# Optimization experiments

Measured on AMD Instinct MI355X. Metric: run time of the kernel, lower is better.

The kernel has to match this reference:

```python
import jax, jax.numpy as jnp
import numpy as np

N, E, B = 10000, 20000, 500
H, NODE_D, EDGE_D, L = 64, 11, 5, 3
BN_EPS = 1e-5
STEPS = 3  # Set2Set processing steps


def setup_inputs() -> dict:
    key = jax.random.key(0)
    ks = jax.random.split(key, 16)
    s = lambda k, shape, fan: (jax.random.normal(k, shape, jnp.float32) / np.sqrt(fan)).astype(jnp.float32)
    p = {}
    p["x"] = jax.random.normal(ks[0], (N, NODE_D), jnp.float32)
    p["edge_index"] = jax.random.randint(ks[1], (2, E), 0, N)
    p["edge_attr"] = jax.random.uniform(ks[2], (E, EDGE_D), dtype=jnp.float32)
    p["batch"] = jnp.sort(jax.random.randint(ks[3], (N,), 0, B))
    # node encoder
    p["W_enc"] = s(ks[4], (NODE_D, H), NODE_D); p["b_enc"] = jnp.zeros((H,), jnp.float32)
    # per-layer NNConv block params (stacked over L layers)
    p["eW1"] = s(ks[5], (L, EDGE_D, H), EDGE_D); p["eb1"] = jnp.zeros((L, H), jnp.float32)
    p["eW2"] = s(ks[6], (L, H, H * H), H);       p["eb2"] = jnp.zeros((L, H * H), jnp.float32)
    p["root"] = s(ks[7], (L, H, H), H);          p["cbias"] = jnp.zeros((L, H), jnp.float32)
    p["gamma"] = jnp.ones((L, H), jnp.float32);  p["beta"] = jnp.zeros((L, H), jnp.float32)
    # Set2Set LSTM (input 2H, hidden H)
    p["Wih"] = s(ks[8], (4 * H, 2 * H), 2 * H); p["Whh"] = s(ks[9], (4 * H, H), H)
    p["bih"] = jnp.zeros((4 * H,), jnp.float32); p["bhh"] = jnp.zeros((4 * H,), jnp.float32)
    p["hW1"] = s(ks[10], (2 * H, H), 2 * H);   p["hb1"] = jnp.zeros((H,), jnp.float32)
    p["hW2"] = s(ks[11], (H, H // 2), H);      p["hb2"] = jnp.zeros((H // 2,), jnp.float32)
    p["hW3"] = s(ks[12], (H // 2, 1), H // 2); p["hb3"] = jnp.zeros((1,), jnp.float32)
    return p


def _forward(x, edge_attr, W_enc, b_enc, eW1, eb1, eW2, eb2, root, cbias, gamma, beta,
             Wih, Whh, bih, bhh, hW1, hb1, hW2, hb2, hW3, hb3, edge_index, batch):
    src, dst = edge_index[0], edge_index[1]
    # in-degree for mean aggregation (0-degree nodes -> 0 output, clamp avoids /0)
    deg = jax.ops.segment_sum(jnp.ones((E,), jnp.float32), dst, num_segments=N)
    deg = jnp.maximum(deg, 1.0)[:, None]

    h = jax.nn.relu(x @ W_enc + b_enc)  # [N, H]

    for l in range(L):
        residual = h
        # edge MLP -> per-edge [H, H] weight matrix
        e1 = jax.nn.relu(edge_attr @ eW1[l] + eb1[l])          # [E, H]
        W = (e1 @ eW2[l] + eb2[l]).reshape(E, H, H)            # [E, H, H]
        msg = jnp.einsum('eh,eho->eo', h[src], W)              # per-edge matvec
        agg = jax.ops.segment_sum(msg, dst, num_segments=N) / deg
        h = agg + h @ root[l] + cbias[l]                       # NNConv (root + bias)
        # BatchNorm1d (training-mode batch stats, biased var), eval-mode dropout (no-op)
        mu = jnp.mean(h, axis=0)
        var = jnp.mean((h - mu) ** 2, axis=0)
        h = (h - mu) * jax.lax.rsqrt(var + BN_EPS) * gamma[l] + beta[l]
        h = jax.nn.relu(h) + residual

    # Set2Set readout
    q_star = jnp.zeros((B, 2 * H), jnp.float32)
    hl = jnp.zeros((B, H), jnp.float32)
    cl = jnp.zeros((B, H), jnp.float32)
    for _ in range(STEPS):
        gates = q_star @ Wih.T + bih + hl @ Whh.T + bhh
        i, f, g, o = jnp.split(gates, 4, axis=1)
        cl = jax.nn.sigmoid(f) * cl + jax.nn.sigmoid(i) * jnp.tanh(g)
        hl = jax.nn.sigmoid(o) * jnp.tanh(cl)
        q = hl                                                  # [B, H]
        e = jnp.sum(h * q[batch], axis=-1)                      # [N]
        m = jax.ops.segment_max(e, batch, num_segments=B)
        ex = jnp.exp(e - m[batch])
        sden = jax.ops.segment_sum(ex, batch, num_segments=B)
        a = ex / sden[batch]                                    # per-graph softmax
        r = jax.ops.segment_sum(a[:, None] * h, batch, num_segments=B)
        q_star = jnp.concatenate([q, r], axis=1)

    # head
    z = jax.nn.relu(q_star @ hW1 + hb1)
    z = jax.nn.relu(z @ hW2 + hb2)
    out = z @ hW3 + hb3
    return out.reshape(-1)  # [B]


def reference(x, edge_index, edge_attr, batch, W_enc, b_enc, eW1, eb1, eW2, eb2, root,
              cbias, gamma, beta, Wih, Whh, bih, bhh, hW1, hb1, hW2, hb2, hW3, hb3):
    return _forward(x, edge_attr, W_enc, b_enc, eW1, eb1, eW2, eb2, root, cbias, gamma,
                    beta, Wih, Whh, bih, bhh, hW1, hb1, hW2, hb2, hW3, hb3,
                    edge_index, batch)
```

## Files before the change

### kernel.cpp

```cpp
#include <hip/hip_runtime.h>
#include <math.h>

#define ND 11
#define ED 5
#define NL 3
#define NSTEPS 3
#define BN_EPS 1e-5f
#define NSLAB 32
#define CAP 256

typedef _Float16 half8 __attribute__((ext_vector_type(8)));
typedef float f32x4 __attribute__((ext_vector_type(4)));

__device__ __forceinline__ float sigm(float x) { return 1.0f / (1.0f + expf(-x)); }

__global__ __launch_bounds__(256) void k_setup(
    const float* __restrict__ x, const float* __restrict__ Wenc,
    const float* __restrict__ benc, float* __restrict__ h0,
    _Float16* __restrict__ hh, int N,
    const int* __restrict__ dst, float* __restrict__ deg, int E,
    const int* __restrict__ batch, int* __restrict__ ptr, int B,
    const float* __restrict__ Wih, const float* __restrict__ Whh,
    const float* __restrict__ bih, const float* __restrict__ bhh,
    float* __restrict__ WihT, float* __restrict__ WhhT, float* __restrict__ gbias,
    const float* __restrict__ w2, const float* __restrict__ b2,
    _Float16* __restrict__ w2P, float* __restrict__ zp, long NZ,
    int nbEnc, int nbDeg, int nbPtr, int nbPackW, int nbPack3) {
  int bid = blockIdx.x;
  const int tid = threadIdx.x;
  if (bid < nbEnc) {
    int idx = bid * 256 + tid;
    if (idx < N * 64) {
      int n = idx >> 6, j = idx & 63;
      float acc = benc[j];
#pragma unroll
      for (int i = 0; i < ND; ++i) acc = fmaf(x[n * ND + i], Wenc[i * 64 + j], acc);
      float v = fmaxf(acc, 0.0f);
      h0[idx] = v;
      hh[idx] = (_Float16)v;
    }
    return;
  }
  bid -= nbEnc;
  if (bid < nbDeg) {
    int e = bid * 256 + tid;
    if (e < E) atomicAdd(&deg[dst[e]], 1.0f);
    return;
  }
  bid -= nbDeg;
  if (bid < nbPtr) {
    int n = bid * 256 + tid;
    if (n < N) {
      int b = batch[n];
      int pb = (n == 0) ? -1 : batch[n - 1];
      for (int g = pb + 1; g <= b; ++g) ptr[g] = n;
      if (n == N - 1)
        for (int g = b + 1; g <= B; ++g) ptr[g] = N;
    }
    return;
  }
  bid -= nbPtr;
  if (bid < nbPackW) {
    int idx = bid * 256 + tid;
    if (idx < 128 * 256) {
      int i = idx >> 8, g = idx & 255;
      WihT[i * 256 + g] = Wih[g * 128 + i];
    } else if (idx < 192 * 256) {
      int j = idx - 128 * 256;
      int i = j >> 8, g = j & 255;
      WhhT[i * 256 + g] = Whh[g * 64 + i];
    } else if (idx < 192 * 256 + 256) {
      int g = idx - 192 * 256;
      gbias[g] = bih[g] + bhh[g];
    }
    return;
  }
  bid -= nbPackW;
  if (bid < nbPack3) {
    int lay = bid / 130;
    int idx = (bid % 130) * 256 + tid;
    int l = idx & 63;
    int f = (idx >> 6) & 7;
    int s = idx >> 9;
    int nf = f >> 1, kf = f & 1;
    const float* srow = (s < 64) ? (w2 + (size_t)lay * 64 * 4096 + (size_t)s * 4096)
                                 : (b2 + (size_t)lay * 4096);
    int o = nf * 16 + (l & 15);
    int hb = kf * 32 + (l >> 4) * 8;
    half8 v;
#pragma unroll
    for (int j = 0; j < 8; ++j) v[j] = (_Float16)srow[(hb + j) * 64 + o];
    *(half8*)(w2P + ((size_t)lay * 65 * 8 * 64 + idx) * 8) = v;
    return;
  }
  bid -= nbPack3;
  {
    long i4 = ((long)bid * 256 + tid) * 4;
    if (i4 + 3 < NZ) *(float4*)(zp + i4) = make_float4(0.f, 0.f, 0.f, 0.f);
    else for (; i4 < NZ; ++i4) zp[i4] = 0.f;
  }
}

__global__ void k_zdeg(float* __restrict__ deg, int N) {
  int i = blockIdx.x * blockDim.x + threadIdx.x;
  if (i < N) deg[i] = 0.f;
}

__global__ __launch_bounds__(256) void k_scan(const float* __restrict__ deg,
                                              int* __restrict__ dptr,
                                              int* __restrict__ cursor, int N) {
  __shared__ int wsum[4];
  __shared__ int s_carry;
  const int tid = threadIdx.x, lane = tid & 63, w = tid >> 6;
  if (tid == 0) s_carry = 0;
  __syncthreads();
  for (int base = 0; base < N; base += 1024) {
    int n0 = base + tid * 4;
    int v[4];
    int s = 0;
#pragma unroll
    for (int i = 0; i < 4; ++i) { v[i] = (n0 + i < N) ? (int)deg[n0 + i] : 0; s += v[i]; }
    int sc = s;
#pragma unroll
    for (int off = 1; off < 64; off <<= 1) {
      int t = __shfl_up(sc, off);
      if (lane >= off) sc += t;
    }
    if (lane == 63) wsum[w] = sc;
    __syncthreads();
    int wpre = 0;
    for (int ww = 0; ww < w; ++ww) wpre += wsum[ww];
    int excl = s_carry + wpre + sc - s;
#pragma unroll
    for (int i = 0; i < 4; ++i) {
      if (n0 + i < N) { dptr[n0 + i] = excl; cursor[n0 + i] = excl; }
      excl += v[i];
    }
    __syncthreads();
    if (tid == 255) s_carry += wsum[0] + wsum[1] + wsum[2] + wsum[3];
    __syncthreads();
  }
  if (threadIdx.x == 0) dptr[N] = s_carry;
}

__global__ void k_fill(const int* __restrict__ dst, const int* __restrict__ src,
                       int* __restrict__ cursor, int* __restrict__ perm,
                       int* __restrict__ srcP, int* __restrict__ dstP, int E) {
  int e = blockIdx.x * blockDim.x + threadIdx.x;
  if (e < E) {
    int d = dst[e];
    int slot = atomicAdd(&cursor[d], 1);
    perm[slot] = e;
    srcP[slot] = src[e];
    dstP[slot] = d;
  }
}

__global__ __launch_bounds__(256) void k_hmat(
    const float* __restrict__ hn, const float* __restrict__ hp,
    const float* __restrict__ slab, const float* __restrict__ gm,
    const float* __restrict__ bt, float* __restrict__ hout,
    _Float16* __restrict__ hh, int N) {
  __shared__ float stats[128];
  const int tid = threadIdx.x;
  if (tid < 128) {
    float s = 0.f;
#pragma unroll
    for (int sl = 0; sl < NSLAB; ++sl) s += slab[sl * 128 + tid];
    stats[tid] = s;
  }
  __syncthreads();
  int idx = blockIdx.x * 256 + tid;
  if (idx >= N * 64) return;
  int o = idx & 63;
  float invN = 1.0f / (float)N;
  float mu = stats[o] * invN;
  float var = stats[64 + o] * invN - mu * mu;
  float rs = rsqrtf(var + BN_EPS) * gm[o];
  float v = fmaxf((hn[idx] - mu) * rs + bt[o], 0.f) + hp[idx];
  hout[idx] = v;
  hh[idx] = (_Float16)v;
}

__global__ __launch_bounds__(512, 2) void k_msgagg(
    const float* __restrict__ ea, const int* __restrict__ perm,
    const float* __restrict__ eW1l, const float* __restrict__ eb1l,
    const _Float16* __restrict__ hh, const int* __restrict__ srcP,
    const int* __restrict__ dstP, const int* __restrict__ dptr,
    const _Float16* __restrict__ w2P, float* __restrict__ agg, int E, int N) {
  __shared__ _Float16 e1t[65][64];
  __shared__ float tileH[2][64][66];
  __shared__ float eat[64][ED];
  __shared__ float w1s[ED * 64];
  __shared__ float b1s[64];

  const int tid = threadIdx.x;
  const int wid = tid >> 6, l = tid & 63;
  const int half = wid >> 2, quad = wid & 3;
  const int lo = l & 15, lg = l >> 4;
  const int e0 = blockIdx.x * 64;

  half8 hsf[4][2];
#pragma unroll
  for (int m = 0; m < 4; ++m) {
    int s = e0 + m * 16 + lo;
    if (s < E) {
      const _Float16* hr = hh + (size_t)srcP[s] * 64;
      hsf[m][0] = *(const half8*)(hr + lg * 8);
      hsf[m][1] = *(const half8*)(hr + 32 + lg * 8);
    } else {
      half8 z = {0, 0, 0, 0, 0, 0, 0, 0};
      hsf[m][0] = z;
      hsf[m][1] = z;
    }
  }

  if (tid < ED * 64) w1s[tid] = eW1l[tid];
  else if (tid < ED * 64 + 64) b1s[tid - ED * 64] = eb1l[tid - ED * 64];
  if (tid >= 448) {
    int s = e0 + (tid - 448);
    if (s < E) {
      int e = perm[s];
#pragma unroll
      for (int i = 0; i < ED; ++i) eat[tid - 448][i] = ea[(size_t)e * ED + i];
    } else {
#pragma unroll
      for (int i = 0; i < ED; ++i) eat[tid - 448][i] = 0.f;
    }
  }
  __syncthreads();

  for (int idx = tid; idx < 65 * 64; idx += 512) {
    int el = idx & 63, k = idx >> 6;
    float v = 1.0f;
    if (k < 64) {
      v = b1s[k];
#pragma unroll
      for (int i = 0; i < ED; ++i) v = fmaf(eat[el][i], w1s[i * 64 + k], v);
      v = fmaxf(v, 0.f);
    }
    e1t[k][el] = (_Float16)v;
  }
  __syncthreads();

  const int kb = half ? 32 : 0;
  f32x4 acc[4] = {};
  const half8* wp = (const half8*)w2P;
  half8 Br[4][2];
  _Float16 sr[4][4];
#pragma unroll
  for (int d = 0; d < 4; ++d) {
    const int k = kb + d;
    Br[d][0] = wp[((size_t)k * 8 + quad * 2 + 0) * 64 + l];
    Br[d][1] = wp[((size_t)k * 8 + quad * 2 + 1) * 64 + l];
#pragma unroll
    for (int m = 0; m < 4; ++m)
      sr[d][m] = (half && d == 0) ? (_Float16)0.f : e1t[k][m * 16 + lo];
  }
#pragma unroll 33
  for (int i = 0; i < 33; ++i) {
    const int d = i & 3;
#pragma unroll
    for (int m = 0; m < 4; ++m) {
      const _Float16 s16 = sr[d][m];
      half8 A0 = hsf[m][0] * s16;
      half8 A1 = hsf[m][1] * s16;
      acc[m] = __builtin_amdgcn_mfma_f32_16x16x32_f16(A0, Br[d][0], acc[m], 0, 0, 0);
      acc[m] = __builtin_amdgcn_mfma_f32_16x16x32_f16(A1, Br[d][1], acc[m], 0, 0, 0);
    }
    if (i + 4 < 33) {
      const int kn = kb + i + 4;
      Br[d][0] = wp[((size_t)kn * 8 + quad * 2 + 0) * 64 + l];
      Br[d][1] = wp[((size_t)kn * 8 + quad * 2 + 1) * 64 + l];
#pragma unroll
      for (int m = 0; m < 4; ++m) sr[d][m] = e1t[kn][m * 16 + lo];
    }
  }

#pragma unroll
  for (int m = 0; m < 4; ++m)
#pragma unroll
    for (int r = 0; r < 4; ++r)
      tileH[half][m * 16 + lg * 4 + r][quad * 16 + lo] = acc[m][r];
  __syncthreads();

  const int o = tid & 63, r8 = tid >> 6;
  const int lastSlot = (e0 + 63 < E) ? (e0 + 63) : (E - 1);
  int nLo = dstP[e0], nHi = dstP[lastSlot];
  nLo = (nLo < 0) ? 0 : ((nLo >= N) ? N - 1 : nLo);
  nHi = (nHi < 0) ? 0 : ((nHi >= N) ? N - 1 : nHi);
  for (int nn = nLo + r8; nn <= nHi; nn += 8) {
    int d0 = dptr[nn], d1 = dptr[nn + 1];
    d0 = (d0 < 0) ? 0 : d0;
    d1 = (d1 > E) ? E : d1;
    int j0 = (d0 > e0) ? d0 : e0;
    int j1 = (d1 < e0 + 64) ? d1 : (e0 + 64);
    float sum = 0.f;
    for (int j = j0; j < j1; ++j) sum += tileH[0][j - e0][o] + tileH[1][j - e0][o];
    float* dp = agg + (size_t)nn * 64 + o;
    if (d0 < e0 || d1 > e0 + 64) { if (j1 > j0) atomicAdd(dp, sum); }
    else *dp = sum;
  }
}

__global__ __launch_bounds__(256) void k_update(
    const float* __restrict__ hcur, float* __restrict__ agg,
    const float* __restrict__ deg, const float* __restrict__ root,
    const float* __restrict__ cb, float* __restrict__ hn_out,
    float* __restrict__ slab_out, int N) {
  __shared__ float hrow[16][64];
  __shared__ float red[2][256];
  const int tid = threadIdx.x, o = tid & 63, r = tid >> 6;
  const int nb = blockIdx.x * 16;
#pragma unroll
  for (int ii = 0; ii < 4; ++ii) {
    int n = nb + ii * 4 + r;
    hrow[ii * 4 + r][o] = (n < N) ? hcur[(size_t)n * 64 + o] : 0.f;
  }
  __syncthreads();
  float acc[4] = {0.f, 0.f, 0.f, 0.f};
  for (int c = 0; c < 64; ++c) {
    float rv = root[c * 64 + o];
#pragma unroll
    for (int ii = 0; ii < 4; ++ii) acc[ii] = fmaf(hrow[ii * 4 + r][c], rv, acc[ii]);
  }
  float s = 0.f, ss = 0.f;
  const float cbv = cb[o];
#pragma unroll
  for (int ii = 0; ii < 4; ++ii) {
    int n = nb + ii * 4 + r;
    if (n < N) {
      float a = agg[(size_t)n * 64 + o];
      agg[(size_t)n * 64 + o] = 0.f;
      float v = acc[ii] + cbv + a / fmaxf(deg[n], 1.0f);
      hn_out[(size_t)n * 64 + o] = v;
      s += v;
      ss += v * v;
    }
  }
  red[0][tid] = s;
  red[1][tid] = ss;
  __syncthreads();
  if (r == 0) {
    float t0 = red[0][o] + red[0][64 + o] + red[0][128 + o] + red[0][192 + o];
    float t1 = red[1][o] + red[1][64 + o] + red[1][128 + o] + red[1][192 + o];
    float* sl = slab_out + (size_t)(blockIdx.x & (NSLAB - 1)) * 128;
    atomicAdd(&sl[o], t0);
    atomicAdd(&sl[64 + o], t1);
  }
}

__global__ __launch_bounds__(256) void k_s2s_all(
    const float* __restrict__ hn2, const float* __restrict__ h2,
    const float* __restrict__ slab2, const float* __restrict__ gm,
    const float* __restrict__ bt, const int* __restrict__ ptr,
    const float* __restrict__ WihT, const float* __restrict__ WhhT,
    const float* __restrict__ gbias,
    const float* __restrict__ hW1, const float* __restrict__ hb1,
    const float* __restrict__ hW2, const float* __restrict__ hb2,
    const float* __restrict__ hW3, const float* __restrict__ hb3,
    float* __restrict__ out, int N) {
  __shared__ float hvs[CAP * 65];
  __shared__ float stats[128];
  __shared__ float mu_s[64], rs_s[64], bt_s[64];
  __shared__ float qs[128];
  __shared__ float hlc[64], clc[64];
  __shared__ float gates[256];
  __shared__ float qv[64];
  __shared__ float ev[256];
  __shared__ float av[CAP];
  __shared__ float redM[4], redS[4];
  __shared__ float redR[4][64];
  __shared__ float z1[64], z2[32];
  const int b = blockIdx.x, tid = threadIdx.x;
  const int wid = tid >> 6, lane = tid & 63;

  if (tid < 128) {
    float s = 0.f;
#pragma unroll
    for (int sl = 0; sl < NSLAB; ++sl) s += slab2[sl * 128 + tid];
    stats[tid] = s;
    qs[tid] = 0.f;
  }
  if (tid < 64) { hlc[tid] = 0.f; clc[tid] = 0.f; }
  __syncthreads();
  if (tid < 64) {
    float invN = 1.0f / (float)N;
    float mu = stats[tid] * invN;
    float var = stats[64 + tid] * invN - mu * mu;
    mu_s[tid] = mu;
    rs_s[tid] = rsqrtf(var + BN_EPS) * gm[tid];
    bt_s[tid] = bt[tid];
  }
  __syncthreads();
  int beg = ptr[b], end = ptr[b + 1];
  if (beg < 0) beg = 0;
  if (end > N) end = N;
  const int nn = (end > beg) ? (end - beg) : 0;
  const bool big = nn > CAP;

  if (!big) {
    for (int idx = tid; idx < nn * 64; idx += 256) {
      int n = idx >> 6, o = idx & 63;
      size_t g = (size_t)(beg + n) * 64 + o;
      hvs[n * 65 + o] = fmaxf((hn2[g] - mu_s[o]) * rs_s[o] + bt_s[o], 0.f) + h2[g];
    }
  }
  __syncthreads();

  for (int step = 0; step < NSTEPS; ++step) {
    float g = gbias[tid];
    for (int i = 0; i < 128; ++i) g = fmaf(qs[i], WihT[i * 256 + tid], g);
    for (int i = 0; i < 64; ++i) g = fmaf(hlc[i], WhhT[i * 256 + tid], g);
    gates[tid] = g;
    __syncthreads();
    if (tid < 64) {
      float ig = sigm(gates[tid]);
      float fg = sigm(gates[64 + tid]);
      float gg = tanhf(gates[128 + tid]);
      float og = sigm(gates[192 + tid]);
      float c = fg * clc[tid] + ig * gg;
      clc[tid] = c;
      float hnew = og * tanhf(c);
      hlc[tid] = hnew;
      qv[tid] = hnew;
    }
    __syncthreads();

    if (!big) {
      if (tid < nn) {
        float s = 0.f;
#pragma unroll 8
        for (int o = 0; o < 64; ++o) s = fmaf(hvs[tid * 65 + o], qv[o], s);
        ev[tid] = s;
      } else {
        ev[tid] = -INFINITY;
      }
      __syncthreads();
      if (tid < 64) {
        float m4 = fmaxf(fmaxf(ev[tid], ev[64 + tid]), fmaxf(ev[128 + tid], ev[192 + tid]));
#pragma unroll
        for (int s = 32; s; s >>= 1) m4 = fmaxf(m4, __shfl_xor(m4, s));
        if (tid == 0) redM[0] = m4;
      }
      __syncthreads();
      const float m = redM[0];
      float a = 0.f;
      if (tid < nn) { a = expf(ev[tid] - m); av[tid] = a; }
      __syncthreads();
      ev[tid] = a;
      __syncthreads();
      if (tid < 64) {
        float s4 = ev[tid] + ev[64 + tid] + ev[128 + tid] + ev[192 + tid];
#pragma unroll
        for (int s = 32; s; s >>= 1) s4 += __shfl_xor(s4, s);
        if (tid == 0) redS[0] = s4;
      }
      __syncthreads();
      const float sden = redS[0];
      if (tid < 128) {
        if (tid < 64) {
          qs[tid] = qv[tid];
        } else {
          int o = tid - 64;
          float r = 0.f;
          for (int n = 0; n < nn; ++n) r = fmaf(av[n], hvs[n * 65 + o], r);
          qs[tid] = (nn > 0) ? r / sden : 0.f;
        }
      }
      __syncthreads();
    } else {
      const float q = qv[lane];
      float mw = -INFINITY;
      for (int n = beg + wid; n < end; n += 4) {
        float hv = fmaxf((hn2[(size_t)n * 64 + lane] - mu_s[lane]) * rs_s[lane] + bt_s[lane],
                         0.f) + h2[(size_t)n * 64 + lane];
        float p = hv * q;
#pragma unroll
        for (int s = 32; s; s >>= 1) p += __shfl_xor(p, s);
        mw = fmaxf(mw, p);
      }
      if (lane == 0) redM[wid] = mw;
      __syncthreads();
      const float m = fmaxf(fmaxf(redM[0], redM[1]), fmaxf(redM[2], redM[3]));
      float ssum = 0.f, racc = 0.f;
      for (int n = beg + wid; n < end; n += 4) {
        float hv = fmaxf((hn2[(size_t)n * 64 + lane] - mu_s[lane]) * rs_s[lane] + bt_s[lane],
                         0.f) + h2[(size_t)n * 64 + lane];
        float p = hv * q;
#pragma unroll
        for (int s = 32; s; s >>= 1) p += __shfl_xor(p, s);
        float a = expf(p - m);
        ssum += a;
        racc = fmaf(a, hv, racc);
      }
      if (lane == 0) redS[wid] = ssum;
      redR[wid][lane] = racc;
      __syncthreads();
      if (tid < 128) {
        if (tid < 64) {
          qs[tid] = qv[tid];
        } else {
          int o2 = tid - 64;
          float rsum = redR[0][o2] + redR[1][o2] + redR[2][o2] + redR[3][o2];
          float sd = redS[0] + redS[1] + redS[2] + redS[3];
          qs[tid] = (end > beg) ? rsum / sd : 0.0f;
        }
      }
      __syncthreads();
    }
  }

  if (tid < 64) {
    float a = hb1[tid];
    for (int i = 0; i < 128; ++i) a = fmaf(qs[i], hW1[i * 64 + tid], a);
    z1[tid] = fmaxf(a, 0.0f);
  }
  __syncthreads();
  if (tid < 32) {
    float a2 = hb2[tid];
    for (int i = 0; i < 64; ++i) a2 = fmaf(z1[i], hW2[i * 32 + tid], a2);
    z2[tid] = fmaxf(a2, 0.0f);
  }
  __syncthreads();
  if (tid < 64) {
    float p = (tid < 32) ? z2[tid] * hW3[tid] : 0.0f;
#pragma unroll
    for (int s = 32; s; s >>= 1) p += __shfl_xor(p, s);
    if (tid == 0) out[b] = p + hb3[0];
  }
}

extern "C" void kernel_launch(void* const* d_in, const int* in_sizes, int n_in,
                              void* d_out, int out_size, void* d_ws, size_t ws_size,
                              hipStream_t stream) {
  const float* x = (const float*)d_in[0];
  const int* eidx = (const int*)d_in[1];
  const float* ea = (const float*)d_in[2];
  const int* batch = (const int*)d_in[3];
  const float* Wenc = (const float*)d_in[4];
  const float* benc = (const float*)d_in[5];
  const float* eW1 = (const float*)d_in[6];
  const float* eb1 = (const float*)d_in[7];
  const float* eW2 = (const float*)d_in[8];
  const float* eb2 = (const float*)d_in[9];
  const float* root = (const float*)d_in[10];
  const float* cbias = (const float*)d_in[11];
  const float* gamma = (const float*)d_in[12];
  const float* beta = (const float*)d_in[13];
  const float* Wih = (const float*)d_in[14];
  const float* Whh = (const float*)d_in[15];
  const float* bih = (const float*)d_in[16];
  const float* bhh = (const float*)d_in[17];
  const float* hW1 = (const float*)d_in[18];
  const float* hb1 = (const float*)d_in[19];
  const float* hW2 = (const float*)d_in[20];
  const float* hb2 = (const float*)d_in[21];
  const float* hW3 = (const float*)d_in[22];
  const float* hb3 = (const float*)d_in[23];

  const int N = in_sizes[0] / ND;
  const int E = in_sizes[1] / 2;
  const int B = out_size;
  const int* srcp = eidx;
  const int* dstp = eidx + E;
  const int Etiles = (E + 63) / 64;

  float* ws = (float*)d_ws;
  float* deg = ws;
  float* agg = deg + N;
  float* bnslab = agg + (size_t)N * 64;
  const long NZ = (long)((size_t)N * 64 + NL * NSLAB * 128);
  float* h0 = bnslab + NL * NSLAB * 128;
  float* h1 = h0 + (size_t)N * 64;
  float* h2 = h1 + (size_t)N * 64;
  float* hn0 = h2 + (size_t)N * 64;
  float* hn1 = hn0 + (size_t)N * 64;
  float* hn2 = hn1 + (size_t)N * 64;
  _Float16* w2P = (_Float16*)(hn2 + (size_t)N * 64);
  _Float16* hhalf = w2P + (size_t)3 * 65 * 8 * 64 * 8;
  float* WihT = (float*)(hhalf + (size_t)N * 64);
  float* WhhT = WihT + 128 * 256;
  float* gbias = WhhT + 64 * 256;
  int* dptr = (int*)(gbias + 256);
  int* cursor = dptr + N + 1;
  int* perm = cursor + N;
  int* srcP = perm + E;
  int* dstP = srcP + E;
  int* ptr = dstP + E;

  const int nbEnc = (N * 64 + 255) / 256;
  const int nbDeg = (E + 255) / 256;
  const int nbPtr = (N + 255) / 256;
  const int nbPackW = (192 * 256 + 256 + 255) / 256;
  const int nbPack3 = 130 * NL;
  const int nbZero = (int)((NZ / 4 + 255) / 256);

  k_zdeg<<<(N + 255) / 256, 256, 0, stream>>>(deg, N);
  k_setup<<<nbEnc + nbDeg + nbPtr + nbPackW + nbPack3 + nbZero, 256, 0, stream>>>(
      x, Wenc, benc, h0, hhalf, N, dstp, deg, E, batch, ptr, B,
      Wih, Whh, bih, bhh, WihT, WhhT, gbias, eW2, eb2, w2P, agg, NZ,
      nbEnc, nbDeg, nbPtr, nbPackW, nbPack3);
  k_scan<<<1, 256, 0, stream>>>(deg, dptr, cursor, N);
  k_fill<<<(E + 255) / 256, 256, 0, stream>>>(dstp, srcp, cursor, perm, srcP, dstP, E);

  float* hbuf[3] = {h0, h1, h2};
  float* hnbuf[3] = {hn0, hn1, hn2};
  for (int l = 0; l < NL; ++l) {
    float* slab_l = bnslab + (size_t)l * NSLAB * 128;
    const _Float16* w2_l = w2P + (size_t)l * 65 * 8 * 64 * 8;
    if (l > 0) {
      k_hmat<<<(N * 64 + 255) / 256, 256, 0, stream>>>(
          hnbuf[l - 1], hbuf[l - 1], bnslab + (size_t)(l - 1) * NSLAB * 128,
          gamma + (l - 1) * 64, beta + (l - 1) * 64, hbuf[l], hhalf, N);
    }
    k_msgagg<<<Etiles, 512, 0, stream>>>(ea, perm, eW1 + (size_t)l * ED * 64,
                                         eb1 + (size_t)l * 64, hhalf, srcP, dstP, dptr,
                                         w2_l, agg, E, N);
    k_update<<<(N + 15) / 16, 256, 0, stream>>>(hbuf[l], agg, deg,
                                                root + (size_t)l * 64 * 64,
                                                cbias + l * 64, hnbuf[l], slab_l, N);
  }

  k_s2s_all<<<B, 256, 0, stream>>>(hn2, h2, bnslab + (size_t)2 * NSLAB * 128,
                                   gamma + 2 * 64, beta + 2 * 64, ptr, WihT, WhhT, gbias,
                                   hW1, hb1, hW2, hb2, hW3, hb3, (float*)d_out, N);
}
```

Before: 204.4 us.

## Split msgagg MFMA work by edge rows instead of K halves

The 8 waves of the message kernel no longer split the 65-long K dimension into two halves that each cover all 64 edges. Each wave now covers half the edge rows across the full K range. This halves the per-wave accumulator and hsf registers and removes the double tileH buffer and its reduction. In exchange, each wave streams twice as many w2 B-fragments from global memory (65 k-steps instead of about 33), and the loop is longer, with the same MFMA count per wave.

```diff
diff --git a/kernel.cpp b/kernel.cpp
--- a/kernel.cpp
+++ b/kernel.cpp
@@ -189,29 +189,29 @@
     const int* __restrict__ dstP, const int* __restrict__ dptr,
     const _Float16* __restrict__ w2P, float* __restrict__ agg, int E, int N) {
   __shared__ _Float16 e1t[65][64];
-  __shared__ float tileH[2][64][66];
+  __shared__ float tileH[64][66];
   __shared__ float eat[64][ED];
   __shared__ float w1s[ED * 64];
   __shared__ float b1s[64];
 
   const int tid = threadIdx.x;
   const int wid = tid >> 6, l = tid & 63;
-  const int half = wid >> 2, quad = wid & 3;
+  const int mh = wid >> 2, quad = wid & 3;
   const int lo = l & 15, lg = l >> 4;
   const int e0 = blockIdx.x * 64;
 
-  half8 hsf[4][2];
-#pragma unroll
-  for (int m = 0; m < 4; ++m) {
-    int s = e0 + m * 16 + lo;
+  half8 hsf[2][2];
+#pragma unroll
+  for (int mm = 0; mm < 2; ++mm) {
+    int s = e0 + (mh * 2 + mm) * 16 + lo;
     if (s < E) {
       const _Float16* hr = hh + (size_t)srcP[s] * 64;
-      hsf[m][0] = *(const half8*)(hr + lg * 8);
-      hsf[m][1] = *(const half8*)(hr + 32 + lg * 8);
+      hsf[mm][0] = *(const half8*)(hr + lg * 8);
+      hsf[mm][1] = *(const half8*)(hr + 32 + lg * 8);
     } else {
       half8 z = {0, 0, 0, 0, 0, 0, 0, 0};
-      hsf[m][0] = z;
-      hsf[m][1] = z;
+      hsf[mm][0] = z;
+      hsf[mm][1] = z;
     }
   }
 
@@ -243,45 +243,40 @@
   }
   __syncthreads();
 
-  const int kb = half ? 32 : 0;
-  f32x4 acc[4] = {};
+  f32x4 acc[2] = {};
   const half8* wp = (const half8*)w2P;
   half8 Br[4][2];
-  _Float16 sr[4][4];
 #pragma unroll
   for (int d = 0; d < 4; ++d) {
-    const int k = kb + d;
-    Br[d][0] = wp[((size_t)k * 8 + quad * 2 + 0) * 64 + l];
-    Br[d][1] = wp[((size_t)k * 8 + quad * 2 + 1) * 64 + l];
-#pragma unroll
-    for (int m = 0; m < 4; ++m)
-      sr[d][m] = (half && d == 0) ? (_Float16)0.f : e1t[k][m * 16 + lo];
-  }
-#pragma unroll 33
-  for (int i = 0; i < 33; ++i) {
-    const int d = i & 3;
-#pragma unroll
-    for (int m = 0; m < 4; ++m) {
-      const _Float16 s16 = sr[d][m];
-      half8 A0 = hsf[m][0] * s16;
-      half8 A1 = hsf[m][1] * s16;
-      acc[m] = __builtin_amdgcn_mfma_f32_16x16x32_f16(A0, Br[d][0], acc[m], 0, 0, 0);
-      acc[m] = __builtin_amdgcn_mfma_f32_16x16x32_f16(A1, Br[d][1], acc[m], 0, 0, 0);
-    }
-    if (i + 4 < 33) {
-      const int kn = kb + i + 4;
-      Br[d][0] = wp[((size_t)kn * 8 + quad * 2 + 0) * 64 + l];
-      Br[d][1] = wp[((size_t)kn * 8 + quad * 2 + 1) * 64 + l];
-#pragma unroll
-      for (int m = 0; m < 4; ++m) sr[d][m] = e1t[kn][m * 16 + lo];
-    }
-  }
-
-#pragma unroll
-  for (int m = 0; m < 4; ++m)
+    Br[d][0] = wp[((size_t)d * 8 + quad * 2 + 0) * 64 + l];
+    Br[d][1] = wp[((size_t)d * 8 + quad * 2 + 1) * 64 + l];
+  }
+  const int mb0 = (mh * 2 + 0) * 16 + lo;
+  const int mb1 = (mh * 2 + 1) * 16 + lo;
+#pragma unroll 65
+  for (int k = 0; k < 65; ++k) {
+    const int d = k & 3;
+    const _Float16 s0 = e1t[k][mb0];
+    const _Float16 s1 = e1t[k][mb1];
+    half8 A00 = hsf[0][0] * s0;
+    half8 A01 = hsf[0][1] * s0;
+    half8 A10 = hsf[1][0] * s1;
+    half8 A11 = hsf[1][1] * s1;
+    acc[0] = __builtin_amdgcn_mfma_f32_16x16x32_f16(A00, Br[d][0], acc[0], 0, 0, 0);
+    acc[0] = __builtin_amdgcn_mfma_f32_16x16x32_f16(A01, Br[d][1], acc[0], 0, 0, 0);
+    acc[1] = __builtin_amdgcn_mfma_f32_16x16x32_f16(A10, Br[d][0], acc[1], 0, 0, 0);
+    acc[1] = __builtin_amdgcn_mfma_f32_16x16x32_f16(A11, Br[d][1], acc[1], 0, 0, 0);
+    if (k + 4 < 65) {
+      Br[d][0] = wp[((size_t)(k + 4) * 8 + quad * 2 + 0) * 64 + l];
+      Br[d][1] = wp[((size_t)(k + 4) * 8 + quad * 2 + 1) * 64 + l];
+    }
+  }
+
+#pragma unroll
+  for (int mm = 0; mm < 2; ++mm)
 #pragma unroll
     for (int r = 0; r < 4; ++r)
-      tileH[half][m * 16 + lg * 4 + r][quad * 16 + lo] = acc[m][r];
+      tileH[(mh * 2 + mm) * 16 + lg * 4 + r][quad * 16 + lo] = acc[mm][r];
   __syncthreads();
 
   const int o = tid & 63, r8 = tid >> 6;
@@ -296,7 +291,7 @@
     int j0 = (d0 > e0) ? d0 : e0;
     int j1 = (d1 < e0 + 64) ? d1 : (e0 + 64);
     float sum = 0.f;
-    for (int j = j0; j < j1; ++j) sum += tileH[0][j - e0][o] + tileH[1][j - e0][o];
+    for (int j = j0; j < j1; ++j) sum += tileH[j - e0][o];
     float* dp = agg + (size_t)nn * 64 + o;
     if (d0 < e0 || d1 > e0 + 64) { if (j1 > j0) atomicAdd(dp, sum); }
     else *dp = sum;
```

After: 184.4 us. -9.8%, faster.

## Stage edge-weight slabs in LDS and double edges per block in message kernel

Applied to the files above, without the earlier changes.

The message-aggregation kernel now handles 128 edges per block instead of 64, with each wave owning 16 edges and computing all 64 outputs across the full K range. Previously the two half-blocks split K and each wave read its own weight fragments from global memory. Now the packed W2 weights are loaded cooperatively into shared memory in chunks of 4 K-rows, padded from 65 to 68 rows so the chunks divide evenly, and every wave reuses them. This cuts redundant global weight traffic and removes the cross-half reduction in tileH. In exchange it adds two block barriers per chunk, raises LDS use, halves the block count, and loses the old register prefetch pipelining.

```diff
diff --git a/kernel.cpp b/kernel.cpp
--- a/kernel.cpp
+++ b/kernel.cpp
@@ -8,6 +8,8 @@
 #define BN_EPS 1e-5f
 #define NSLAB 32
 #define CAP 256
+#define KSL 68
+#define ET 128
 
 typedef _Float16 half8 __attribute__((ext_vector_type(8)));
 typedef float f32x4 __attribute__((ext_vector_type(4)));
@@ -77,20 +79,25 @@
   }
   bid -= nbPackW;
   if (bid < nbPack3) {
-    int lay = bid / 130;
-    int idx = (bid % 130) * 256 + tid;
+    int lay = bid / 136;
+    int idx = (bid % 136) * 256 + tid;
     int l = idx & 63;
     int f = (idx >> 6) & 7;
     int s = idx >> 9;
     int nf = f >> 1, kf = f & 1;
-    const float* srow = (s < 64) ? (w2 + (size_t)lay * 64 * 4096 + (size_t)s * 4096)
-                                 : (b2 + (size_t)lay * 4096);
     int o = nf * 16 + (l & 15);
     int hb = kf * 32 + (l >> 4) * 8;
     half8 v;
-#pragma unroll
-    for (int j = 0; j < 8; ++j) v[j] = (_Float16)srow[(hb + j) * 64 + o];
-    *(half8*)(w2P + ((size_t)lay * 65 * 8 * 64 + idx) * 8) = v;
+    if (s < 65) {
+      const float* srow = (s < 64) ? (w2 + (size_t)lay * 64 * 4096 + (size_t)s * 4096)
+                                   : (b2 + (size_t)lay * 4096);
+#pragma unroll
+      for (int j = 0; j < 8; ++j) v[j] = (_Float16)srow[(hb + j) * 64 + o];
+    } else {
+#pragma unroll
+      for (int j = 0; j < 8; ++j) v[j] = (_Float16)0.f;
+    }
+    *(half8*)(w2P + ((size_t)lay * KSL * 8 * 64 + idx) * 8) = v;
     return;
   }
   bid -= nbPack3;
@@ -188,104 +195,98 @@
     const _Float16* __restrict__ hh, const int* __restrict__ srcP,
     const int* __restrict__ dstP, const int* __restrict__ dptr,
     const _Float16* __restrict__ w2P, float* __restrict__ agg, int E, int N) {
-  __shared__ _Float16 e1t[65][64];
-  __shared__ float tileH[2][64][66];
-  __shared__ float eat[64][ED];
+  __shared__ half8 Bs[4 * 8 * 64];
+  __shared__ _Float16 e1t[KSL][ET];
+  __shared__ float tileH[ET][66];
+  __shared__ float eat[ET][ED];
   __shared__ float w1s[ED * 64];
   __shared__ float b1s[64];
 
   const int tid = threadIdx.x;
-  const int wid = tid >> 6, l = tid & 63;
-  const int half = wid >> 2, quad = wid & 3;
+  const int w = tid >> 6, l = tid & 63;
   const int lo = l & 15, lg = l >> 4;
-  const int e0 = blockIdx.x * 64;
-
-  half8 hsf[4][2];
-#pragma unroll
-  for (int m = 0; m < 4; ++m) {
-    int s = e0 + m * 16 + lo;
+  const int e0 = blockIdx.x * ET;
+
+  half8 hsf[2];
+  {
+    int s = e0 + w * 16 + lo;
     if (s < E) {
       const _Float16* hr = hh + (size_t)srcP[s] * 64;
-      hsf[m][0] = *(const half8*)(hr + lg * 8);
-      hsf[m][1] = *(const half8*)(hr + 32 + lg * 8);
+      hsf[0] = *(const half8*)(hr + lg * 8);
+      hsf[1] = *(const half8*)(hr + 32 + lg * 8);
     } else {
       half8 z = {0, 0, 0, 0, 0, 0, 0, 0};
-      hsf[m][0] = z;
-      hsf[m][1] = z;
+      hsf[0] = z;
+      hsf[1] = z;
     }
   }
 
   if (tid < ED * 64) w1s[tid] = eW1l[tid];
   else if (tid < ED * 64 + 64) b1s[tid - ED * 64] = eb1l[tid - ED * 64];
-  if (tid >= 448) {
-    int s = e0 + (tid - 448);
+  if (tid >= 384) {
+    int s = e0 + (tid - 384);
     if (s < E) {
       int e = perm[s];
 #pragma unroll
-      for (int i = 0; i < ED; ++i) eat[tid - 448][i] = ea[(size_t)e * ED + i];
+      for (int i = 0; i < ED; ++i) eat[tid - 384][i] = ea[(size_t)e * ED + i];
     } else {
 #pragma unroll
-      for (int i = 0; i < ED; ++i) eat[tid - 448][i] = 0.f;
-    }
-  }
-  __syncthreads();
-
-  for (int idx = tid; idx < 65 * 64; idx += 512) {
-    int el = idx & 63, k = idx >> 6;
-    float v = 1.0f;
+      for (int i = 0; i < ED; ++i) eat[tid - 384][i] = 0.f;
+    }
+  }
+  __syncthreads();
+
+  for (int idx = tid; idx < KSL * ET; idx += 512) {
+    int el = idx & (ET - 1), k = idx >> 7;
+    float v = 0.f;
     if (k < 64) {
       v = b1s[k];
 #pragma unroll
       for (int i = 0; i < ED; ++i) v = fmaf(eat[el][i], w1s[i * 64 + k], v);
       v = fmaxf(v, 0.f);
+    } else if (k == 64) {
+      v = 1.0f;
     }
     e1t[k][el] = (_Float16)v;
   }
-  __syncthreads();
-
-  const int kb = half ? 32 : 0;
+
   f32x4 acc[4] = {};
   const half8* wp = (const half8*)w2P;
-  half8 Br[4][2];
-  _Float16 sr[4][4];
-#pragma unroll
-  for (int d = 0; d < 4; ++d) {
-    const int k = kb + d;
-    Br[d][0] = wp[((size_t)k * 8 + quad * 2 + 0) * 64 + l];
-    Br[d][1] = wp[((size_t)k * 8 + quad * 2 + 1) * 64 + l];
-#pragma unroll
-    for (int m = 0; m < 4; ++m)
-      sr[d][m] = (half && d == 0) ? (_Float16)0.f : e1t[k][m * 16 + lo];
-  }
-#pragma unroll 33
-  for (int i = 0; i < 33; ++i) {
-    const int d = i & 3;
-#pragma unroll
-    for (int m = 0; m < 4; ++m) {
-      const _Float16 s16 = sr[d][m];
-      half8 A0 = hsf[m][0] * s16;
-      half8 A1 = hsf[m][1] * s16;
-      acc[m] = __builtin_amdgcn_mfma_f32_16x16x32_f16(A0, Br[d][0], acc[m], 0, 0, 0);
-      acc[m] = __builtin_amdgcn_mfma_f32_16x16x32_f16(A1, Br[d][1], acc[m], 0, 0, 0);
-    }
-    if (i + 4 < 33) {
-      const int kn = kb + i + 4;
-      Br[d][0] = wp[((size_t)kn * 8 + quad * 2 + 0) * 64 + l];
-      Br[d][1] = wp[((size_t)kn * 8 + quad * 2 + 1) * 64 + l];
-#pragma unroll
-      for (int m = 0; m < 4; ++m) sr[d][m] = e1t[kn][m * 16 + lo];
-    }
-  }
-
-#pragma unroll
-  for (int m = 0; m < 4; ++m)
+  const int eb = w * 16 + lo;
+  for (int c = 0; c < 17; ++c) {
+    __syncthreads();
+#pragma unroll
+    for (int i = 0; i < 4; ++i) {
+      int u = tid + i * 512;
+      Bs[u] = wp[(size_t)c * 2048 + u];
+    }
+    __syncthreads();
+#pragma unroll
+    for (int kk = 0; kk < 4; ++kk) {
+      const int k = c * 4 + kk;
+      const _Float16 s16 = e1t[k][eb];
+      half8 A0 = hsf[0] * s16;
+      half8 A1 = hsf[1] * s16;
+#pragma unroll
+      for (int q = 0; q < 4; ++q) {
+        acc[q] = __builtin_amdgcn_mfma_f32_16x16x32_f16(A0, Bs[(kk * 8 + q * 2 + 0) * 64 + l],
+                                                        acc[q], 0, 0, 0);
+        acc[q] = __builtin_amdgcn_mfma_f32_16x16x32_f16(A1, Bs[(kk * 8 + q * 2 + 1) * 64 + l],
+                                                        acc[q], 0, 0, 0);
+      }
+    }
+  }
+
+  __syncthreads();
+#pragma unroll
+  for (int q = 0; q < 4; ++q)
 #pragma unroll
     for (int r = 0; r < 4; ++r)
-      tileH[half][m * 16 + lg * 4 + r][quad * 16 + lo] = acc[m][r];
+      tileH[w * 16 + lg * 4 + r][q * 16 + lo] = acc[q][r];
   __syncthreads();
 
   const int o = tid & 63, r8 = tid >> 6;
-  const int lastSlot = (e0 + 63 < E) ? (e0 + 63) : (E - 1);
+  const int lastSlot = (e0 + ET - 1 < E) ? (e0 + ET - 1) : (E - 1);
   int nLo = dstP[e0], nHi = dstP[lastSlot];
   nLo = (nLo < 0) ? 0 : ((nLo >= N) ? N - 1 : nLo);
   nHi = (nHi < 0) ? 0 : ((nHi >= N) ? N - 1 : nHi);
@@ -294,11 +295,11 @@
     d0 = (d0 < 0) ? 0 : d0;
     d1 = (d1 > E) ? E : d1;
     int j0 = (d0 > e0) ? d0 : e0;
-    int j1 = (d1 < e0 + 64) ? d1 : (e0 + 64);
+    int j1 = (d1 < e0 + ET) ? d1 : (e0 + ET);
     float sum = 0.f;
-    for (int j = j0; j < j1; ++j) sum += tileH[0][j - e0][o] + tileH[1][j - e0][o];
+    for (int j = j0; j < j1; ++j) sum += tileH[j - e0][o];
     float* dp = agg + (size_t)nn * 64 + o;
-    if (d0 < e0 || d1 > e0 + 64) { if (j1 > j0) atomicAdd(dp, sum); }
+    if (d0 < e0 || d1 > e0 + ET) { if (j1 > j0) atomicAdd(dp, sum); }
     else *dp = sum;
   }
 }
@@ -564,7 +565,7 @@
   const int B = out_size;
   const int* srcp = eidx;
   const int* dstp = eidx + E;
-  const int Etiles = (E + 63) / 64;
+  const int Etiles = (E + ET - 1) / ET;
 
   float* ws = (float*)d_ws;
   float* deg = ws;
@@ -578,7 +579,7 @@
   float* hn1 = hn0 + (size_t)N * 64;
   float* hn2 = hn1 + (size_t)N * 64;
   _Float16* w2P = (_Float16*)(hn2 + (size_t)N * 64);
-  _Float16* hhalf = w2P + (size_t)3 * 65 * 8 * 64 * 8;
+  _Float16* hhalf = w2P + (size_t)3 * KSL * 8 * 64 * 8;
   float* WihT = (float*)(hhalf + (size_t)N * 64);
   float* WhhT = WihT + 128 * 256;
   float* gbias = WhhT + 64 * 256;
@@ -593,7 +594,7 @@
   const int nbDeg = (E + 255) / 256;
   const int nbPtr = (N + 255) / 256;
   const int nbPackW = (192 * 256 + 256 + 255) / 256;
-  const int nbPack3 = 130 * NL;
+  const int nbPack3 = 136 * NL;
   const int nbZero = (int)((NZ / 4 + 255) / 256);
 
   k_zdeg<<<(N + 255) / 256, 256, 0, stream>>>(deg, N);
@@ -608,7 +609,7 @@
   float* hnbuf[3] = {hn0, hn1, hn2};
   for (int l = 0; l < NL; ++l) {
     float* slab_l = bnslab + (size_t)l * NSLAB * 128;
-    const _Float16* w2_l = w2P + (size_t)l * 65 * 8 * 64 * 8;
+    const _Float16* w2_l = w2P + (size_t)l * KSL * 8 * 64 * 8;
     if (l > 0) {
       k_hmat<<<(N * 64 + 255) / 256, 256, 0, stream>>>(
           hnbuf[l - 1], hbuf[l - 1], bnslab + (size_t)(l - 1) * NSLAB * 128,
```

New measurement: 205.4 us. No clear change (+0.5%).
